# Kernel tuning notes

Hardware: AMD Instinct MI355X
Metric: run time of the kernel (lower is better)

Reference implementation:

```python
import jax, jax.numpy as jnp
import numpy as np

N_NODES = 50000
N_EDGES = 800000
F_X = 128
F_E = 128
HID = 256
F_OUT = 128


def setup_inputs() -> dict:
    key = jax.random.key(0)
    k1, k2, k3, k4, k5 = jax.random.split(key, 5)
    x = jax.random.normal(k1, (N_NODES, F_X), dtype=jnp.float32)
    edge_index = jax.random.randint(k2, (2, N_EDGES), 0, N_NODES, dtype=jnp.int64)
    edge_attr = jax.random.normal(k3, (N_EDGES, F_E), dtype=jnp.float32)
    din = F_X + F_E
    W1 = jax.random.normal(k4, (din, HID), dtype=jnp.float32) * (1.0 / np.sqrt(din))
    b1 = jnp.zeros((HID,), dtype=jnp.float32)
    W2 = jax.random.normal(k5, (HID, F_OUT), dtype=jnp.float32) * (1.0 / np.sqrt(HID))
    b2 = jnp.zeros((F_OUT,), dtype=jnp.float32)
    return {"x": x, "edge_index": edge_index, "edge_attr": edge_attr,
            "W1": W1, "b1": b1, "W2": W2, "b2": b2}


def reference(x, edge_index, edge_attr, W1, b1, W2, b2):
    num_nodes = x.shape[0]
    dst = edge_index[1]
    # scatter-mean of edge_attr onto destination nodes
    sums = jax.ops.segment_sum(edge_attr, dst, num_segments=num_nodes)  # [N, F_e]
    ones = jnp.ones((edge_attr.shape[0],), dtype=edge_attr.dtype)
    counts = jax.ops.segment_sum(ones, dst, num_segments=num_nodes)  # [N]
    agg = sums / jnp.maximum(counts, 1.0)[:, None]
    node_inputs = jnp.concatenate([x, agg], axis=-1)  # [N, F_x+F_e]
    h = jax.nn.relu(node_inputs @ W1 + b1)
    return h @ W2 + b2
```

## Files before the change

### kernel.cpp

```cpp
#include <hip/hip_runtime.h>

#define N_NODES 50000
#define N_EDGES 800000
#define F_E     128
#define HID     256
#define F_OUT   128
#define DIN     256
#define LDA     264
#define TILE_M  32
#define CAP     96
#define PREP_BLOCKS ((DIN * HID + HID * F_OUT) / 256)
#define FILL_BLOCKS (N_EDGES / 4 / 256)

typedef __attribute__((ext_vector_type(8))) short short8;
typedef __attribute__((ext_vector_type(4))) float f32x4;

__device__ __forceinline__ unsigned short f2bf(float f) {
    unsigned int u = __float_as_uint(f);
    u = u + 0x7FFFu + ((u >> 16) & 1u);
    return (unsigned short)(u >> 16);
}

__global__ __launch_bounds__(256) void combo_kernel(const void* ei,
                                                    const float* __restrict__ W1,
                                                    const float* __restrict__ W2,
                                                    unsigned short* __restrict__ W1T,
                                                    unsigned short* __restrict__ W2T,
                                                    int* __restrict__ counts,
                                                    int* __restrict__ slots) {
    const int tid = threadIdx.x;
    if (blockIdx.x < PREP_BLOCKS) {
        int idx = blockIdx.x * 256 + tid;
        if (idx < DIN * HID) {
            int j = idx & 255, k = idx >> 8;
            W1T[j * 256 + k] = f2bf(W1[k * 256 + j]);
        } else {
            int t = idx - DIN * HID;
            int j = t & 127, k = t >> 7;
            W2T[j * 256 + k] = f2bf(W2[k * 128 + j]);
        }
        return;
    }
    const int lane = tid & 63;
    const unsigned int* w = (const unsigned int*)ei;
    unsigned int oddacc = 0;
#pragma unroll
    for (int k = 0; k < 4; ++k) oddacc |= w[2 * (lane * 4 + k) + 1];
    const int is64 = (__ballot(oddacc != 0u) == 0ULL);

    const int e = ((int)blockIdx.x - PREP_BLOCKS) * 1024 + tid * 4;
    if (e >= N_EDGES) return;
    int d[4];
    if (is64) {
        const long long* p = (const long long*)ei + N_EDGES + e;
        longlong2 a = *(const longlong2*)p;
        longlong2 b = *(const longlong2*)(p + 2);
        d[0] = (int)a.x; d[1] = (int)a.y; d[2] = (int)b.x; d[3] = (int)b.y;
    } else {
        int4 q = *(const int4*)((const int*)ei + N_EDGES + e);
        d[0] = q.x; d[1] = q.y; d[2] = q.z; d[3] = q.w;
    }
#pragma unroll
    for (int j = 0; j < 4; ++j) {
        int pos = atomicAdd(&counts[d[j]], 1);
        if (pos < CAP) slots[d[j] * CAP + pos] = e + j;
    }
}

__global__ __launch_bounds__(256) void fused_mlp_kernel(const float* __restrict__ x,
                                                        const float* __restrict__ edge_attr,
                                                        const int* __restrict__ counts,
                                                        const int* __restrict__ slots,
                                                        const unsigned short* __restrict__ W1T,
                                                        const float* __restrict__ b1,
                                                        const unsigned short* __restrict__ W2T,
                                                        const float* __restrict__ b2,
                                                        float* __restrict__ out) {
    __shared__ short A_lds[TILE_M * LDA];
    const int tid  = threadIdx.x;
    const int base = blockIdx.x * TILE_M;
    const int lane = tid & 63;
    const int wid  = tid >> 6;
    const int h    = lane >> 5;
    const int c    = lane & 31;

#pragma unroll
    for (int t = 0; t < 4; ++t) {
        const int nrow = wid * 8 + t * 2 + h;
        const int node = base + nrow;
        float4 xv = make_float4(0.f, 0.f, 0.f, 0.f);
        if (node < N_NODES) xv = *(const float4*)&x[node * 128 + 4 * c];
        *(ushort4*)&A_lds[nrow * LDA + 4 * c] =
            make_ushort4(f2bf(xv.x), f2bf(xv.y), f2bf(xv.z), f2bf(xv.w));
    }

    for (int nn = 0; nn < 8; ++nn) {
        const int nrow = wid * 8 + nn;
        const int node = base + nrow;
        int cnt = 0;
        if (node < N_NODES) {
            cnt = counts[node];
            cnt = cnt < CAP ? cnt : CAP;
        }
        const int beg = node * CAP;
        f32x4 acc = {0.f, 0.f, 0.f, 0.f};
        for (int p = 0; p < cnt; p += 16) {
            int eid[8];
#pragma unroll
            for (int j = 0; j < 8; ++j) {
                int q = p + 2 * j + h;
                q = q < cnt - 1 ? q : cnt - 1;
                eid[j] = slots[beg + q];
            }
            f32x4 v[8];
#pragma unroll
            for (int j = 0; j < 8; ++j)
                v[j] = *(const f32x4*)&edge_attr[(size_t)eid[j] * F_E + 4 * c];
#pragma unroll
            for (int j = 0; j < 8; ++j)
                if (p + 2 * j + h < cnt) acc += v[j];
        }
#pragma unroll
        for (int k = 0; k < 4; ++k) acc[k] += __shfl_xor(acc[k], 32);
        const float inv = 1.0f / (float)(cnt > 0 ? cnt : 1);
        if (h == 0)
            *(ushort4*)&A_lds[nrow * LDA + 128 + 4 * c] =
                make_ushort4(f2bf(acc[0] * inv), f2bf(acc[1] * inv),
                             f2bf(acc[2] * inv), f2bf(acc[3] * inv));
    }
    __syncthreads();

    const int lr = lane & 15;
    const int lg = lane >> 4;
    const int wc = wid * 64;

    f32x4 acc[2][4] = {};
#pragma unroll
    for (int kb = 0; kb < 8; ++kb) {
        short8 af[2];
#pragma unroll
        for (int m = 0; m < 2; ++m)
            af[m] = *(const short8*)&A_lds[(m * 16 + lr) * LDA + kb * 32 + lg * 8];
        short8 bf[4];
#pragma unroll
        for (int n = 0; n < 4; ++n)
            bf[n] = *(const short8*)&W1T[(wc + n * 16 + lr) * 256 + kb * 32 + lg * 8];
#pragma unroll
        for (int m = 0; m < 2; ++m)
#pragma unroll
            for (int n = 0; n < 4; ++n)
                acc[m][n] = __builtin_amdgcn_mfma_f32_16x16x32_bf16(af[m], bf[n], acc[m][n], 0, 0, 0);
    }

    float b1v[4];
#pragma unroll
    for (int n = 0; n < 4; ++n) b1v[n] = b1[wc + n * 16 + lr];

    __syncthreads();
#pragma unroll
    for (int m = 0; m < 2; ++m)
#pragma unroll
        for (int n = 0; n < 4; ++n)
#pragma unroll
            for (int i = 0; i < 4; ++i) {
                float hh = acc[m][n][i] + b1v[n];
                hh = hh > 0.f ? hh : 0.f;
                A_lds[(m * 16 + lg * 4 + i) * LDA + wc + n * 16 + lr] = (short)f2bf(hh);
            }
    __syncthreads();

    const int wc2 = wid * 32;
    f32x4 acc2[2][2] = {};
#pragma unroll
    for (int kb = 0; kb < 8; ++kb) {
        short8 af[2];
#pragma unroll
        for (int m = 0; m < 2; ++m)
            af[m] = *(const short8*)&A_lds[(m * 16 + lr) * LDA + kb * 32 + lg * 8];
        short8 bf[2];
#pragma unroll
        for (int n = 0; n < 2; ++n)
            bf[n] = *(const short8*)&W2T[(wc2 + n * 16 + lr) * 256 + kb * 32 + lg * 8];
#pragma unroll
        for (int m = 0; m < 2; ++m)
#pragma unroll
            for (int n = 0; n < 2; ++n)
                acc2[m][n] = __builtin_amdgcn_mfma_f32_16x16x32_bf16(af[m], bf[n], acc2[m][n], 0, 0, 0);
    }

    float b2v[2];
#pragma unroll
    for (int n = 0; n < 2; ++n) b2v[n] = b2[wc2 + n * 16 + lr];
#pragma unroll
    for (int m = 0; m < 2; ++m)
#pragma unroll
        for (int n = 0; n < 2; ++n)
#pragma unroll
            for (int i = 0; i < 4; ++i) {
                int node = base + m * 16 + lg * 4 + i;
                if (node < N_NODES)
                    out[node * F_OUT + wc2 + n * 16 + lr] = acc2[m][n][i] + b2v[n];
            }
}

extern "C" void kernel_launch(void* const* d_in, const int* in_sizes, int n_in,
                              void* d_out, int out_size, void* d_ws, size_t ws_size,
                              hipStream_t stream) {
    const float* x         = (const float*)d_in[0];
    const void*  ei        = d_in[1];
    const float* edge_attr = (const float*)d_in[2];
    const float* W1        = (const float*)d_in[3];
    const float* b1        = (const float*)d_in[4];
    const float* W2        = (const float*)d_in[5];
    const float* b2        = (const float*)d_in[6];
    float* out = (float*)d_out;

    char* ws = (char*)d_ws;
    size_t off = 0;
    auto alloc = [&](size_t bytes) -> void* {
        void* p = ws + off;
        off = (off + bytes + 255) & ~(size_t)255;
        return p;
    };
    int*            counts = (int*)alloc((size_t)N_NODES * 4);
    int*            slots  = (int*)alloc((size_t)N_NODES * CAP * 4);
    unsigned short* w1t    = (unsigned short*)alloc((size_t)DIN * HID * 2);
    unsigned short* w2t    = (unsigned short*)alloc((size_t)HID * F_OUT * 2);
    (void)ws_size; (void)in_sizes; (void)n_in; (void)out_size;

    hipMemsetAsync(counts, 0, (size_t)N_NODES * 4, stream);
    const int fill_blocks = (N_EDGES / 4 + 255) / 256;
    combo_kernel<<<PREP_BLOCKS + fill_blocks, 256, 0, stream>>>(ei, W1, W2, w1t, w2t,
                                                                counts, slots);
    fused_mlp_kernel<<<(N_NODES + TILE_M - 1) / TILE_M, 256, 0, stream>>>(
        x, edge_attr, counts, slots, w1t, b1, w2t, b2, out);
}
```

Before: 209.4 us.

## Merge fill and MLP kernels into one persistent kernel with grid barrier

```diff
diff --git a/kernel.cpp b/kernel.cpp
--- a/kernel.cpp
+++ b/kernel.cpp
@@ -7,10 +7,10 @@
 #define F_OUT   128
 #define DIN     256
 #define LDA     264
-#define TILE_M  32
+#define TILE_M  64
 #define CAP     96
-#define PREP_BLOCKS ((DIN * HID + HID * F_OUT) / 256)
-#define FILL_BLOCKS (N_EDGES / 4 / 256)
+#define NB      ((N_NODES + TILE_M - 1) / TILE_M)
+#define NPERSIST 512
 
 typedef __attribute__((ext_vector_type(8))) short short8;
 typedef __attribute__((ext_vector_type(4))) float f32x4;
@@ -21,186 +21,213 @@
     return (unsigned short)(u >> 16);
 }
 
-__global__ __launch_bounds__(256) void combo_kernel(const void* ei,
-                                                    const float* __restrict__ W1,
-                                                    const float* __restrict__ W2,
-                                                    unsigned short* __restrict__ W1T,
-                                                    unsigned short* __restrict__ W2T,
-                                                    int* __restrict__ counts,
-                                                    int* __restrict__ slots) {
-    const int tid = threadIdx.x;
-    if (blockIdx.x < PREP_BLOCKS) {
-        int idx = blockIdx.x * 256 + tid;
-        if (idx < DIN * HID) {
-            int j = idx & 255, k = idx >> 8;
-            W1T[j * 256 + k] = f2bf(W1[k * 256 + j]);
-        } else {
-            int t = idx - DIN * HID;
-            int j = t & 127, k = t >> 7;
-            W2T[j * 256 + k] = f2bf(W2[k * 128 + j]);
-        }
-        return;
-    }
-    const int lane = tid & 63;
-    const unsigned int* w = (const unsigned int*)ei;
-    unsigned int oddacc = 0;
-#pragma unroll
-    for (int k = 0; k < 4; ++k) oddacc |= w[2 * (lane * 4 + k) + 1];
-    const int is64 = (__ballot(oddacc != 0u) == 0ULL);
-
-    const int e = ((int)blockIdx.x - PREP_BLOCKS) * 1024 + tid * 4;
-    if (e >= N_EDGES) return;
-    int d[4];
-    if (is64) {
-        const long long* p = (const long long*)ei + N_EDGES + e;
-        longlong2 a = *(const longlong2*)p;
-        longlong2 b = *(const longlong2*)(p + 2);
-        d[0] = (int)a.x; d[1] = (int)a.y; d[2] = (int)b.x; d[3] = (int)b.y;
-    } else {
-        int4 q = *(const int4*)((const int*)ei + N_EDGES + e);
-        d[0] = q.x; d[1] = q.y; d[2] = q.z; d[3] = q.w;
-    }
-#pragma unroll
-    for (int j = 0; j < 4; ++j) {
-        int pos = atomicAdd(&counts[d[j]], 1);
-        if (pos < CAP) slots[d[j] * CAP + pos] = e + j;
-    }
-}
-
-__global__ __launch_bounds__(256) void fused_mlp_kernel(const float* __restrict__ x,
-                                                        const float* __restrict__ edge_attr,
-                                                        const int* __restrict__ counts,
-                                                        const int* __restrict__ slots,
-                                                        const unsigned short* __restrict__ W1T,
-                                                        const float* __restrict__ b1,
-                                                        const unsigned short* __restrict__ W2T,
-                                                        const float* __restrict__ b2,
-                                                        float* __restrict__ out) {
+__global__ __launch_bounds__(256, 2) void mono_kernel(const void* __restrict__ ei,
+                                                      const float* __restrict__ x,
+                                                      const float* __restrict__ edge_attr,
+                                                      const float* __restrict__ W1,
+                                                      const float* __restrict__ b1,
+                                                      const float* __restrict__ W2,
+                                                      const float* __restrict__ b2,
+                                                      unsigned short* __restrict__ W1T,
+                                                      unsigned short* __restrict__ W2T,
+                                                      int* __restrict__ counts,
+                                                      int* __restrict__ slots,
+                                                      int* __restrict__ bar,
+                                                      float* __restrict__ out) {
     __shared__ short A_lds[TILE_M * LDA];
     const int tid  = threadIdx.x;
-    const int base = blockIdx.x * TILE_M;
+    const int blk  = blockIdx.x;
     const int lane = tid & 63;
     const int wid  = tid >> 6;
     const int h    = lane >> 5;
     const int c    = lane & 31;
 
-#pragma unroll
-    for (int t = 0; t < 4; ++t) {
-        const int nrow = wid * 8 + t * 2 + h;
-        const int node = base + nrow;
-        float4 xv = make_float4(0.f, 0.f, 0.f, 0.f);
-        if (node < N_NODES) xv = *(const float4*)&x[node * 128 + 4 * c];
-        *(ushort4*)&A_lds[nrow * LDA + 4 * c] =
-            make_ushort4(f2bf(xv.x), f2bf(xv.y), f2bf(xv.z), f2bf(xv.w));
-    }
-
-    for (int nn = 0; nn < 8; ++nn) {
-        const int nrow = wid * 8 + nn;
-        const int node = base + nrow;
-        int cnt = 0;
-        if (node < N_NODES) {
-            cnt = counts[node];
-            cnt = cnt < CAP ? cnt : CAP;
-        }
-        const int beg = node * CAP;
-        f32x4 acc = {0.f, 0.f, 0.f, 0.f};
-        for (int p = 0; p < cnt; p += 16) {
-            int eid[8];
-#pragma unroll
-            for (int j = 0; j < 8; ++j) {
-                int q = p + 2 * j + h;
-                q = q < cnt - 1 ? q : cnt - 1;
-                eid[j] = slots[beg + q];
-            }
-            f32x4 v[8];
-#pragma unroll
-            for (int j = 0; j < 8; ++j)
-                v[j] = *(const f32x4*)&edge_attr[(size_t)eid[j] * F_E + 4 * c];
-#pragma unroll
-            for (int j = 0; j < 8; ++j)
-                if (p + 2 * j + h < cnt) acc += v[j];
-        }
-#pragma unroll
-        for (int k = 0; k < 4; ++k) acc[k] += __shfl_xor(acc[k], 32);
-        const float inv = 1.0f / (float)(cnt > 0 ? cnt : 1);
-        if (h == 0)
-            *(ushort4*)&A_lds[nrow * LDA + 128 + 4 * c] =
-                make_ushort4(f2bf(acc[0] * inv), f2bf(acc[1] * inv),
-                             f2bf(acc[2] * inv), f2bf(acc[3] * inv));
+    {
+        const int base = blk * TILE_M;
+#pragma unroll
+        for (int t = 0; t < 8; ++t) {
+            const int nrow = wid * 16 + t * 2 + h;
+            const int node = base + nrow;
+            float4 xv = make_float4(0.f, 0.f, 0.f, 0.f);
+            if (node < N_NODES) xv = *(const float4*)&x[node * 128 + 4 * c];
+            *(ushort4*)&A_lds[nrow * LDA + 4 * c] =
+                make_ushort4(f2bf(xv.x), f2bf(xv.y), f2bf(xv.z), f2bf(xv.w));
+        }
+    }
+
+    {
+        const int idx = blk * 256 + tid;
+        if (idx < DIN * HID) {
+            const int j = idx & 255, k = idx >> 8;
+            W1T[j * 256 + k] = f2bf(W1[k * 256 + j]);
+        } else if (idx < DIN * HID + HID * F_OUT) {
+            const int t2 = idx - DIN * HID;
+            const int j = t2 & 127, k = t2 >> 7;
+            W2T[j * 256 + k] = f2bf(W2[k * 128 + j]);
+        }
+    }
+
+    {
+        const unsigned int* w = (const unsigned int*)ei;
+        unsigned int oddacc = 0;
+#pragma unroll
+        for (int k = 0; k < 4; ++k) oddacc |= w[2 * (lane * 4 + k) + 1];
+        const int is64 = (__ballot(oddacc != 0u) == 0ULL);
+
+        for (int sweep = 0; sweep < 2; ++sweep) {
+            const int e = (sweep * NPERSIST + blk) * 1024 + tid * 4;
+            if (e < N_EDGES) {
+                int d[4];
+                if (is64) {
+                    const long long* p = (const long long*)ei + N_EDGES + e;
+                    longlong2 a = *(const longlong2*)p;
+                    longlong2 b = *(const longlong2*)(p + 2);
+                    d[0] = (int)a.x; d[1] = (int)a.y; d[2] = (int)b.x; d[3] = (int)b.y;
+                } else {
+                    int4 q = *(const int4*)((const int*)ei + N_EDGES + e);
+                    d[0] = q.x; d[1] = q.y; d[2] = q.z; d[3] = q.w;
+                }
+#pragma unroll
+                for (int j = 0; j < 4; ++j) {
+                    int pos = atomicAdd(&counts[d[j]], 1);
+                    if (pos < CAP) slots[d[j] * CAP + pos] = e + j;
+                }
+            }
+        }
+    }
+
+    __syncthreads();
+    if (tid == 0) {
+        __hip_atomic_fetch_add(bar, 1, __ATOMIC_ACQ_REL, __HIP_MEMORY_SCOPE_AGENT);
+        while (__hip_atomic_load(bar, __ATOMIC_ACQUIRE, __HIP_MEMORY_SCOPE_AGENT) < NPERSIST)
+            __builtin_amdgcn_s_sleep(2);
     }
     __syncthreads();
 
     const int lr = lane & 15;
     const int lg = lane >> 4;
-    const int wc = wid * 64;
-
-    f32x4 acc[2][4] = {};
-#pragma unroll
-    for (int kb = 0; kb < 8; ++kb) {
-        short8 af[2];
-#pragma unroll
-        for (int m = 0; m < 2; ++m)
-            af[m] = *(const short8*)&A_lds[(m * 16 + lr) * LDA + kb * 32 + lg * 8];
-        short8 bf[4];
-#pragma unroll
-        for (int n = 0; n < 4; ++n)
-            bf[n] = *(const short8*)&W1T[(wc + n * 16 + lr) * 256 + kb * 32 + lg * 8];
-#pragma unroll
-        for (int m = 0; m < 2; ++m)
+    const int wc  = wid * 64;
+    const int wc2 = wid * 32;
+
+    for (int tile = blk; tile < NB; tile += NPERSIST) {
+        const int base = tile * TILE_M;
+
+        if (tile != blk) {
+            __syncthreads();
+#pragma unroll
+            for (int t = 0; t < 8; ++t) {
+                const int nrow = wid * 16 + t * 2 + h;
+                const int node = base + nrow;
+                float4 xv = make_float4(0.f, 0.f, 0.f, 0.f);
+                if (node < N_NODES) xv = *(const float4*)&x[node * 128 + 4 * c];
+                *(ushort4*)&A_lds[nrow * LDA + 4 * c] =
+                    make_ushort4(f2bf(xv.x), f2bf(xv.y), f2bf(xv.z), f2bf(xv.w));
+            }
+        }
+
+        for (int nn = 0; nn < 16; ++nn) {
+            const int nrow = wid * 16 + nn;
+            const int node = base + nrow;
+            int cnt = 0;
+            if (node < N_NODES) {
+                cnt = counts[node];
+                cnt = cnt < CAP ? cnt : CAP;
+            }
+            const int beg = node * CAP;
+            f32x4 acc = {0.f, 0.f, 0.f, 0.f};
+            for (int p = 0; p < cnt; p += 16) {
+                int eid[8];
+#pragma unroll
+                for (int j = 0; j < 8; ++j) {
+                    int q = p + 2 * j + h;
+                    q = q < cnt - 1 ? q : cnt - 1;
+                    eid[j] = slots[beg + q];
+                }
+                f32x4 v[8];
+#pragma unroll
+                for (int j = 0; j < 8; ++j)
+                    v[j] = *(const f32x4*)&edge_attr[(size_t)eid[j] * F_E + 4 * c];
+#pragma unroll
+                for (int j = 0; j < 8; ++j)
+                    if (p + 2 * j + h < cnt) acc += v[j];
+            }
+#pragma unroll
+            for (int k = 0; k < 4; ++k) acc[k] += __shfl_xor(acc[k], 32);
+            const float inv = 1.0f / (float)(cnt > 0 ? cnt : 1);
+            if (h == 0)
+                *(ushort4*)&A_lds[nrow * LDA + 128 + 4 * c] =
+                    make_ushort4(f2bf(acc[0] * inv), f2bf(acc[1] * inv),
+                                 f2bf(acc[2] * inv), f2bf(acc[3] * inv));
+        }
+        __syncthreads();
+
+        f32x4 acc[4][4] = {};
+#pragma unroll
+        for (int kb = 0; kb < 8; ++kb) {
+            short8 af[4];
+#pragma unroll
+            for (int m = 0; m < 4; ++m)
+                af[m] = *(const short8*)&A_lds[(m * 16 + lr) * LDA + kb * 32 + lg * 8];
+            short8 bf[4];
 #pragma unroll
             for (int n = 0; n < 4; ++n)
-                acc[m][n] = __builtin_amdgcn_mfma_f32_16x16x32_bf16(af[m], bf[n], acc[m][n], 0, 0, 0);
-    }
-
-    float b1v[4];
-#pragma unroll
-    for (int n = 0; n < 4; ++n) b1v[n] = b1[wc + n * 16 + lr];
-
-    __syncthreads();
-#pragma unroll
-    for (int m = 0; m < 2; ++m)
-#pragma unroll
-        for (int n = 0; n < 4; ++n)
-#pragma unroll
-            for (int i = 0; i < 4; ++i) {
-                float hh = acc[m][n][i] + b1v[n];
-                hh = hh > 0.f ? hh : 0.f;
-                A_lds[(m * 16 + lg * 4 + i) * LDA + wc + n * 16 + lr] = (short)f2bf(hh);
-            }
-    __syncthreads();
-
-    const int wc2 = wid * 32;
-    f32x4 acc2[2][2] = {};
-#pragma unroll
-    for (int kb = 0; kb < 8; ++kb) {
-        short8 af[2];
-#pragma unroll
-        for (int m = 0; m < 2; ++m)
-            af[m] = *(const short8*)&A_lds[(m * 16 + lr) * LDA + kb * 32 + lg * 8];
-        short8 bf[2];
-#pragma unroll
-        for (int n = 0; n < 2; ++n)
-            bf[n] = *(const short8*)&W2T[(wc2 + n * 16 + lr) * 256 + kb * 32 + lg * 8];
-#pragma unroll
-        for (int m = 0; m < 2; ++m)
+                bf[n] = *(const short8*)&W1T[(wc + n * 16 + lr) * 256 + kb * 32 + lg * 8];
+#pragma unroll
+            for (int m = 0; m < 4; ++m)
+#pragma unroll
+                for (int n = 0; n < 4; ++n)
+                    acc[m][n] = __builtin_amdgcn_mfma_f32_16x16x32_bf16(af[m], bf[n], acc[m][n], 0, 0, 0);
+        }
+
+        float b1v[4];
+#pragma unroll
+        for (int n = 0; n < 4; ++n) b1v[n] = b1[wc + n * 16 + lr];
+
+        __syncthreads();
+#pragma unroll
+        for (int m = 0; m < 4; ++m)
+#pragma unroll
+            for (int n = 0; n < 4; ++n)
+#pragma unroll
+                for (int i = 0; i < 4; ++i) {
+                    float hh = acc[m][n][i] + b1v[n];
+                    hh = hh > 0.f ? hh : 0.f;
+                    A_lds[(m * 16 + lg * 4 + i) * LDA + wc + n * 16 + lr] = (short)f2bf(hh);
+                }
+        __syncthreads();
+
+        f32x4 acc2[4][2] = {};
+#pragma unroll
+        for (int kb = 0; kb < 8; ++kb) {
+            short8 af[4];
+#pragma unroll
+            for (int m = 0; m < 4; ++m)
+                af[m] = *(const short8*)&A_lds[(m * 16 + lr) * LDA + kb * 32 + lg * 8];
+            short8 bf[2];
 #pragma unroll
             for (int n = 0; n < 2; ++n)
-                acc2[m][n] = __builtin_amdgcn_mfma_f32_16x16x32_bf16(af[m], bf[n], acc2[m][n], 0, 0, 0);
-    }
-
-    float b2v[2];
-#pragma unroll
-    for (int n = 0; n < 2; ++n) b2v[n] = b2[wc2 + n * 16 + lr];
-#pragma unroll
-    for (int m = 0; m < 2; ++m)
-#pragma unroll
-        for (int n = 0; n < 2; ++n)
-#pragma unroll
-            for (int i = 0; i < 4; ++i) {
-                int node = base + m * 16 + lg * 4 + i;
-                if (node < N_NODES)
-                    out[node * F_OUT + wc2 + n * 16 + lr] = acc2[m][n][i] + b2v[n];
-            }
+                bf[n] = *(const short8*)&W2T[(wc2 + n * 16 + lr) * 256 + kb * 32 + lg * 8];
+#pragma unroll
+            for (int m = 0; m < 4; ++m)
+#pragma unroll
+                for (int n = 0; n < 2; ++n)
+                    acc2[m][n] = __builtin_amdgcn_mfma_f32_16x16x32_bf16(af[m], bf[n], acc2[m][n], 0, 0, 0);
+        }
+
+        float b2v[2];
+#pragma unroll
+        for (int n = 0; n < 2; ++n) b2v[n] = b2[wc2 + n * 16 + lr];
+#pragma unroll
+        for (int m = 0; m < 4; ++m)
+#pragma unroll
+            for (int n = 0; n < 2; ++n)
+#pragma unroll
+                for (int i = 0; i < 4; ++i) {
+                    int node = base + m * 16 + lg * 4 + i;
+                    if (node < N_NODES)
+                        out[node * F_OUT + wc2 + n * 16 + lr] = acc2[m][n][i] + b2v[n];
+                }
+    }
 }
 
 extern "C" void kernel_launch(void* const* d_in, const int* in_sizes, int n_in,
@@ -223,15 +250,13 @@
         return p;
     };
     int*            counts = (int*)alloc((size_t)N_NODES * 4);
+    int*            bar    = (int*)alloc(256);
     int*            slots  = (int*)alloc((size_t)N_NODES * CAP * 4);
     unsigned short* w1t    = (unsigned short*)alloc((size_t)DIN * HID * 2);
     unsigned short* w2t    = (unsigned short*)alloc((size_t)HID * F_OUT * 2);
     (void)ws_size; (void)in_sizes; (void)n_in; (void)out_size;
 
-    hipMemsetAsync(counts, 0, (size_t)N_NODES * 4, stream);
-    const int fill_blocks = (N_EDGES / 4 + 255) / 256;
-    combo_kernel<<<PREP_BLOCKS + fill_blocks, 256, 0, stream>>>(ei, W1, W2, w1t, w2t,
-                                                                counts, slots);
-    fused_mlp_kernel<<<(N_NODES + TILE_M - 1) / TILE_M, 256, 0, stream>>>(
-        x, edge_attr, counts, slots, w1t, b1, w2t, b2, out);
+    hipMemsetAsync(ws, 0, (size_t)((char*)bar - ws) + 256, stream);
+    mono_kernel<<<NPERSIST, 256, 0, stream>>>(ei, x, edge_attr, W1, b1, W2, b2,
+                                              w1t, w2t, counts, slots, bar, out);
 }
```

After: 302.4 us. 1.44x slower.
